# Kernel tuning notes

Measured on AMD Instinct MI355X. Metric: run time of the kernel, lower is better.

## Reference

```python
import jax, jax.numpy as jnp
import numpy as np

B, S, D = 1, 4096, 1024
H, Dh = 16, 64
F = 4096  # mlp_factor * D
EPS = 1e-6


def _ln(x, scale, bias=None):
    m = jnp.mean(x, axis=-1, keepdims=True)
    v = jnp.var(x, axis=-1, keepdims=True)
    y = (x - m) * jax.lax.rsqrt(v + EPS) * scale
    return y + bias if bias is not None else y


def setup_inputs() -> dict:
    key = jax.random.key(0)
    ks = jax.random.split(key, 10)
    lecun = lambda k, shape, fan_in: (jax.random.normal(k, shape, jnp.float32) * (fan_in ** -0.5))
    inp = {
        "x": jax.random.normal(ks[0], (B, S, D), jnp.float32),
        # causal mask, broadcastable to [B, H, S, S]
        "mask": jnp.tril(jnp.ones((S, S), bool))[None, None],
        # PreNorm (TPNorm -> LayerNorm)
        "ln_scale": jnp.ones((D,), jnp.float32),
        "ln_bias": jnp.zeros((D,), jnp.float32),
        # MLP input projection
        "w_in": lecun(ks[1], (D, F), D),
        "b_in": jnp.zeros((F,), jnp.float32),
        # QKV projection
        "wq": lecun(ks[2], (D, H, Dh), D),
        "bq": jnp.zeros((H, Dh), jnp.float32),
        "wk": lecun(ks[3], (D, H, Dh), D),
        "bk": jnp.zeros((H, Dh), jnp.float32),
        "wv": lecun(ks[4], (D, H, Dh), D),
        "bv": jnp.zeros((H, Dh), jnp.float32),
        # qk-norm scales (normalize_qk=True)
        "qn_scale": jnp.ones((Dh,), jnp.float32),
        "kn_scale": jnp.ones((Dh,), jnp.float32),
        # MLP output projection
        "w_mo": lecun(ks[5], (F, D), F),
        "b_mo": jnp.zeros((D,), jnp.float32),
        # Attention output projection
        "w_ao": lecun(ks[6], (H * Dh, D), H * Dh),
        "b_ao": jnp.zeros((D,), jnp.float32),
    }
    return inp


def reference(x, mask, ln_scale, ln_bias, w_in, b_in, wq, bq, wk, bk, wv, bv,
              qn_scale, kn_scale, w_mo, b_mo, w_ao, b_ao):
    residual = x
    xn = _ln(x, ln_scale, ln_bias)

    # fused QKV + MLP-input projections (QKVMLPDenseParallel)
    h = jax.nn.gelu(jnp.einsum("bsd,df->bsf", xn, w_in) + b_in)  # [B,S,F]
    q = jnp.einsum("bsd,dhk->bshk", xn, wq) + bq  # [B,S,H,Dh]
    k = jnp.einsum("bsd,dhk->bshk", xn, wk) + bk
    v = jnp.einsum("bsd,dhk->bshk", xn, wv) + bv
    # normalize_qk: per-head LayerNorm (no bias) on q, k
    q = _ln(q, qn_scale)
    k = _ln(k, kn_scale)

    # dot-product attention
    scores = jnp.einsum("bqhd,bkhd->bhqk", q, k) / np.sqrt(Dh).astype(np.float32)
    scores = jnp.where(mask, scores, jnp.finfo(scores.dtype).min)
    attn = jax.nn.softmax(scores, axis=-1)
    o = jnp.einsum("bhqk,bkhd->bqhd", attn, v)  # [B,S,H,Dh]

    # fused attention-out + MLP-out projections (AttnMLPOutParallel)
    mlp_out = jnp.einsum("bsf,fd->bsd", h, w_mo) + b_mo
    attn_out = jnp.einsum("bse,ed->bsd", o.reshape(B, S, H * Dh), w_ao) + b_ao

    # dropout deterministic (train=False); residual add
    return residual + mlp_out + attn_out
```

## Files before the change

kernel.cpp:

```cpp
#include <hip/hip_runtime.h>
#include <hip/hip_fp16.h>

typedef _Float16 half8 __attribute__((ext_vector_type(8)));
typedef float floatx4 __attribute__((ext_vector_type(4)));

constexpr int kS = 4096;
constexpr int kD = 1024;
constexpr int kH = 16;
constexpr int kDh = 64;
constexpr int kF = 4096;
constexpr int kNQKV = kF + 3 * kD;
constexpr int kKOut = kF + kD;

__device__ __forceinline__ void async_ld16(const void* g, void* l) {
  __builtin_amdgcn_global_load_lds(
      (const __attribute__((address_space(1))) void*)g,
      (__attribute__((address_space(3))) void*)l, 16, 0, 0);
}

#define CFENCE() asm volatile("" ::: "memory")

__global__ __launch_bounds__(256) void prep0_kernel(
    const float* __restrict__ w_in, const float* __restrict__ wq,
    const float* __restrict__ wk, const float* __restrict__ wv,
    const float* __restrict__ w_mo, const float* __restrict__ w_ao,
    _Float16* __restrict__ Wqkv, _Float16* __restrict__ Wout,
    const float* __restrict__ x, const float* __restrict__ ln_scale,
    const float* __restrict__ ln_bias, _Float16* __restrict__ xn) {
  __shared__ float t[32][33];
  __shared__ float red[8];
  int id = blockIdx.x;
  const int tid = threadIdx.x;

  if (id >= 12288) {
    const int row = id - 12288;
    const float* xr = x + (size_t)row * kD;
    float v[4];
    float s = 0.f, sq = 0.f;
#pragma unroll
    for (int i = 0; i < 4; ++i) {
      v[i] = xr[tid + 256 * i];
      s += v[i];
      sq += v[i] * v[i];
    }
    for (int off = 32; off; off >>= 1) {
      s += __shfl_xor(s, off);
      sq += __shfl_xor(sq, off);
    }
    const int wv2 = tid >> 6;
    if ((tid & 63) == 0) { red[wv2] = s; red[wv2 + 4] = sq; }
    __syncthreads();
    s = red[0] + red[1] + red[2] + red[3];
    sq = red[4] + red[5] + red[6] + red[7];
    const float mean = s * (1.0f / kD);
    const float var = sq * (1.0f / kD) - mean * mean;
    const float rstd = rsqrtf(var + 1e-6f);
#pragma unroll
    for (int i = 0; i < 4; ++i) {
      int d = tid + 256 * i;
      xn[(size_t)row * kD + d] = (_Float16)((v[i] - mean) * rstd * ln_scale[d] + ln_bias[d]);
    }
    return;
  }

  const float* src; _Float16* dst; int N, ldk, noff, koff, nt, kt;
  if (id < 4096)       { src = w_in; dst = Wqkv; N = kF; ldk = kD; noff = 0;        koff = 0;  nt = id & 127; kt = id >> 7; }
  else if (id < 5120)  { id -= 4096; src = wq;  dst = Wqkv; N = kD; ldk = kD; noff = kF;       koff = 0;  nt = id & 31; kt = id >> 5; }
  else if (id < 6144)  { id -= 5120; src = wk;  dst = Wqkv; N = kD; ldk = kD; noff = kF + kD;  koff = 0;  nt = id & 31; kt = id >> 5; }
  else if (id < 7168)  { id -= 6144; src = wv;  dst = Wqkv; N = kD; ldk = kD; noff = kF + 2*kD; koff = 0; nt = id & 31; kt = id >> 5; }
  else if (id < 11264) { id -= 7168; src = w_mo; dst = Wout; N = kD; ldk = kKOut; noff = 0;    koff = 0;  nt = id & 31; kt = id >> 5; }
  else                 { id -= 11264; src = w_ao; dst = Wout; N = kD; ldk = kKOut; noff = 0;   koff = kF; nt = id & 31; kt = id >> 5; }
  const int n0 = nt * 32, k0 = kt * 32;
#pragma unroll
  for (int i = 0; i < 4; ++i) {
    const int kl = (tid >> 5) + i * 8, nl = tid & 31;
    t[kl][nl] = src[(size_t)(k0 + kl) * N + n0 + nl];
  }
  __syncthreads();
#pragma unroll
  for (int i = 0; i < 4; ++i) {
    const int nl = (tid >> 5) + i * 8, kl = tid & 31;
    dst[(size_t)(noff + n0 + nl) * ldk + koff + k0 + kl] = (_Float16)t[kl][nl];
  }
}

__global__ __launch_bounds__(256) void htrans_kernel(
    const _Float16* __restrict__ src, _Float16* __restrict__ dst, int R, int C) {
  __shared__ _Float16 t[32][34];
  const int tid = threadIdx.x;
  const int c0 = blockIdx.x * 32, r0 = blockIdx.y * 32;
#pragma unroll
  for (int i = 0; i < 4; ++i) {
    const int rl = (tid >> 5) + i * 8, cl = tid & 31;
    t[rl][cl] = src[(size_t)(r0 + rl) * C + c0 + cl];
  }
  __syncthreads();
#pragma unroll
  for (int i = 0; i < 4; ++i) {
    const int cl = (tid >> 5) + i * 8, rl = tid & 31;
    dst[(size_t)(c0 + cl) * R + r0 + rl] = t[rl][cl];
  }
}

__device__ __forceinline__ float fast_gelu(float xv) {
  const float z = 0.7978845608028654f * (xv + 0.044715f * xv * xv * xv);
  const float u = exp2f(fminf(2.885390081777927f * z, 80.0f));
  return xv * u / (1.0f + u);
}

__global__ __launch_bounds__(512, 2) void gemm_qkvin(
    const _Float16* __restrict__ A, const _Float16* __restrict__ Bp,
    const float* __restrict__ b_in, const float* __restrict__ bq,
    const float* __restrict__ bk, const float* __restrict__ bv,
    const float* __restrict__ qn_scale, const float* __restrict__ kn_scale,
    _Float16* __restrict__ ho, _Float16* __restrict__ q,
    _Float16* __restrict__ k, _Float16* __restrict__ v) {
  __shared__ alignas(16) _Float16 Ts[65536];

  const int tid = threadIdx.x;
  const int lane = tid & 63;
  const int wave = tid >> 6;
  const int wr = wave >> 2;
  const int wc = wave & 3;
  const int lrow = lane & 15;
  const int quad = lane >> 4;

  int bid = blockIdx.y * 16 + blockIdx.x;
  bid = (bid & 7) * 56 + (bid >> 3);
  const int m0 = (bid & 15) * 256;
  const int n0 = (bid >> 4) * 256;

  const int swz = ((quad ^ (lrow & 3)) << 3);
  const int aoff = (wr * 128 + lrow) * 32 + swz;
  const int boff = 16384 + (wc * 64 + lrow) * 32 + swz;

  const int srow = wave * 32 + (lane >> 2);
  const int scol = (((lane & 3) ^ ((lane >> 2) & 3)) << 3);
  const int sldsl = wave * 1024;

  floatx4 acc[8][4] = {};

  auto stage = [&](int nb, int p, int kb) {
    const int mat = p & 1;
    const int lds0 = nb * 32768 + mat * 16384 + (p >> 1) * 8192 + sldsl;
    const _Float16* g0 = (mat == 0)
        ? A + (size_t)(m0 + srow) * kD + kb + scol
        : Bp + (size_t)(n0 + srow) * kD + kb + scol;
    async_ld16(g0, Ts + lds0);
    async_ld16(g0 + (size_t)16 * kD, Ts + lds0 + 512);
  };

  stage(0, 0, 0);
  stage(0, 1, 0);
  stage(0, 2, 32);
  stage(0, 3, 32);
  asm volatile("s_waitcnt vmcnt(4)" ::: "memory");
  CFENCE(); __builtin_amdgcn_s_barrier(); CFENCE();

  half8 af[8];
  constexpr int NT = kD / 64;
  for (int t = 0; t < NT; ++t) {
    const int cur = t & 1, nb = cur ^ 1;
    const int co = cur * 32768;
    const bool pf = (t + 1 < NT);
    const int kb1 = (t + 1) * 64;

    auto rdA = [&](int ks) {
#pragma unroll
      for (int mi = 0; mi < 8; ++mi)
        af[mi] = *reinterpret_cast<const half8*>(Ts + co + ks * 8192 + aoff + mi * 512);
    };
    auto rdB = [&](int ks, int nf) -> half8 {
      return *reinterpret_cast<const half8*>(Ts + co + ks * 8192 + boff + nf * 512);
    };
    half8 bf0, bf1;

    auto mm2 = [&](int nf0, half8 b0, half8 b1) {
      __builtin_amdgcn_s_setprio(1);
#pragma unroll
      for (int mi = 0; mi < 8; ++mi)
        acc[mi][nf0] = __builtin_amdgcn_mfma_f32_16x16x32_f16(af[mi], b0, acc[mi][nf0], 0, 0, 0);
#pragma unroll
      for (int mi = 0; mi < 8; ++mi)
        acc[mi][nf0 + 1] = __builtin_amdgcn_mfma_f32_16x16x32_f16(af[mi], b1, acc[mi][nf0 + 1], 0, 0, 0);
      __builtin_amdgcn_s_setprio(0);
    };

    rdA(0); bf0 = rdB(0, 0); bf1 = rdB(0, 1);
    if (pf) stage(nb, 0, kb1);
    CFENCE(); __builtin_amdgcn_s_barrier(); CFENCE();
    mm2(0, bf0, bf1);
    CFENCE(); __builtin_amdgcn_s_barrier(); CFENCE();

    bf0 = rdB(0, 2); bf1 = rdB(0, 3);
    if (pf) {
      stage(nb, 1, kb1);
      asm volatile("s_waitcnt vmcnt(4)" ::: "memory");
    } else {
      asm volatile("s_waitcnt vmcnt(0)" ::: "memory");
    }
    CFENCE(); __builtin_amdgcn_s_barrier(); CFENCE();
    mm2(2, bf0, bf1);
    CFENCE(); __builtin_amdgcn_s_barrier(); CFENCE();

    rdA(1); bf0 = rdB(1, 0); bf1 = rdB(1, 1);
    if (pf) stage(nb, 2, kb1 + 32);
    CFENCE(); __builtin_amdgcn_s_barrier(); CFENCE();
    mm2(0, bf0, bf1);
    CFENCE(); __builtin_amdgcn_s_barrier(); CFENCE();

    bf0 = rdB(1, 2); bf1 = rdB(1, 3);
    if (pf) {
      stage(nb, 3, kb1 + 32);
      asm volatile("s_waitcnt vmcnt(4)" ::: "memory");
    }
    CFENCE(); __builtin_amdgcn_s_barrier(); CFENCE();
    mm2(2, bf0, bf1);
    CFENCE(); __builtin_amdgcn_s_barrier(); CFENCE();
  }

  const int nblk0 = n0 + wc * 64;
  const int rbase = m0 + wr * 128 + quad * 4;

  if (nblk0 < kF) {
#pragma unroll
    for (int mi = 0; mi < 8; ++mi) {
      const int gm = rbase + mi * 16;
#pragma unroll
      for (int nf = 0; nf < 4; ++nf) {
        const int gn = nblk0 + nf * 16 + lrow;
        const float bn = b_in[gn];
#pragma unroll
        for (int r = 0; r < 4; ++r)
          ho[(size_t)(gm + r) * kKOut + gn] = (_Float16)fast_gelu(acc[mi][nf][r] + bn);
      }
    }
  } else if (nblk0 >= kF + 2 * kD) {
    const int cb = nblk0 - (kF + 2 * kD);
#pragma unroll
    for (int mi = 0; mi < 8; ++mi) {
      const int gm = rbase + mi * 16;
#pragma unroll
      for (int nf = 0; nf < 4; ++nf) {
        const int col = cb + nf * 16 + lrow;
        const float bn = bv[col];
#pragma unroll
        for (int r = 0; r < 4; ++r)
          v[(size_t)(gm + r) * kD + col] = (_Float16)(acc[mi][nf][r] + bn);
      }
    }
  } else {
    const bool isq = nblk0 < kF + kD;
    const float* nsc = isq ? qn_scale : kn_scale;
    const float* nb2 = isq ? bq : bk;
    const float sm = isq ? 0.18033688f : 1.0f;
    _Float16* dst = isq ? q : k;
    const int col0 = (nblk0 - kF) & (kD - 1);
    float bj[4];
#pragma unroll
    for (int nf = 0; nf < 4; ++nf) bj[nf] = nb2[col0 + nf * 16 + lrow];
#pragma unroll
    for (int mi = 0; mi < 8; ++mi) {
      const int gm = rbase + mi * 16;
#pragma unroll
      for (int r = 0; r < 4; ++r) {
        float vals[4], s1 = 0.f, s2 = 0.f;
#pragma unroll
        for (int nf = 0; nf < 4; ++nf) {
          const float vv = acc[mi][nf][r] + bj[nf];
          vals[nf] = vv; s1 += vv; s2 += vv * vv;
        }
#pragma unroll
        for (int off = 1; off <= 8; off <<= 1) {
          s1 += __shfl_xor(s1, off);
          s2 += __shfl_xor(s2, off);
        }
        const float mean = s1 * (1.0f / 64.0f);
        const float rstd = rsqrtf(s2 * (1.0f / 64.0f) - mean * mean + 1e-6f);
#pragma unroll
        for (int nf = 0; nf < 4; ++nf) {
          const int d = nf * 16 + lrow;
          dst[(size_t)(gm + r) * kD + col0 + d] =
              (_Float16)((vals[nf] - mean) * rstd * nsc[d] * sm);
        }
      }
    }
  }
}

__global__ __launch_bounds__(256) void prep_kernel(
    const float* __restrict__ x, const float* __restrict__ b_mo,
    const float* __restrict__ b_ao, float* __restrict__ out) {
  const int i = blockIdx.x * 256 + threadIdx.x;
  const int d = i & (kD - 1);
  out[i] = x[i] + b_mo[d] + b_ao[d];
}

__global__ __launch_bounds__(256) void gemm_out(
    const _Float16* __restrict__ A, const _Float16* __restrict__ Bp,
    float* __restrict__ out) {
  __shared__ alignas(16) _Float16 Ts[2][16 * 512];

  const int tid = threadIdx.x;
  const int lane = tid & 63;
  const int wave = tid >> 6;
  const int wm = (wave >> 1) * 64;
  const int wn = (wave & 1) * 64;
  const int m0 = blockIdx.x * 128;
  const int n0 = blockIdx.y * 128;
  const int kbeg = blockIdx.z * (kKOut / 2);
  const int kend = kbeg + kKOut / 2;
  const int lrow = lane & 15;
  const int quad = lane >> 4;

  floatx4 acc[4][4] = {};

  auto stage = [&](int buf, int k0) {
#pragma unroll
    for (int i = 0; i < 4; ++i) {
      const int chunk = wave * 4 + i;
      const int r = ((chunk & 7) << 4) + (lane >> 2);
      const int csrc = ((lane & 3) ^ ((r >> 1) & 3)) << 3;
      const _Float16* src = (chunk < 8)
          ? A + (size_t)(m0 + r) * kKOut + k0 + csrc
          : Bp + (size_t)(n0 + r) * kKOut + k0 + csrc;
      async_ld16(src, &Ts[buf][chunk * 512]);
    }
  };

  stage(0, kbeg);
  asm volatile("s_waitcnt vmcnt(0)" ::: "memory");
  __builtin_amdgcn_s_barrier();

  int cur = 0;
  for (int k0 = kbeg; k0 < kend; k0 += 32) {
    if (k0 + 32 < kend) stage(cur ^ 1, k0 + 32);

    const _Float16* As = Ts[cur];
    const _Float16* Bs = Ts[cur] + 8 * 512;
    half8 af[4], bf[4];
#pragma unroll
    for (int i = 0; i < 4; ++i) {
      const int ra = wm + i * 16 + lrow;
      const int rb = wn + i * 16 + lrow;
      af[i] = *reinterpret_cast<const half8*>(&As[ra * 32 + ((quad ^ ((ra >> 1) & 3)) << 3)]);
      bf[i] = *reinterpret_cast<const half8*>(&Bs[rb * 32 + ((quad ^ ((rb >> 1) & 3)) << 3)]);
    }
#pragma unroll
    for (int i = 0; i < 4; ++i)
#pragma unroll
      for (int j = 0; j < 4; ++j)
        acc[i][j] = __builtin_amdgcn_mfma_f32_16x16x32_f16(af[i], bf[j], acc[i][j], 0, 0, 0);

    asm volatile("s_waitcnt vmcnt(0)" ::: "memory");
    __builtin_amdgcn_s_barrier();
    cur ^= 1;
  }

#pragma unroll
  for (int i = 0; i < 4; ++i) {
    const int gm = m0 + wm + i * 16 + quad * 4;
#pragma unroll
    for (int j = 0; j < 4; ++j) {
      const int gn = n0 + wn + j * 16 + lrow;
#pragma unroll
      for (int r = 0; r < 4; ++r)
        atomicAdd(out + (size_t)(gm + r) * kD + gn, acc[i][j][r]);
    }
  }
}

__global__ __launch_bounds__(256) void fattn_kernel(
    const _Float16* __restrict__ Q, const _Float16* __restrict__ K,
    const _Float16* __restrict__ Vt, _Float16* __restrict__ ho) {
  __shared__ alignas(16) _Float16 Qs[64 * 64];
  __shared__ alignas(16) _Float16 Ks[64 * 64];
  __shared__ alignas(16) _Float16 Vs[64 * 64];
  __shared__ alignas(16) _Float16 Ps[64 * 72];

  const int tid = threadIdx.x;
  const int lane = tid & 63;
  const int wave = tid >> 6;
  const int lrow = lane & 15;
  const int quad = lane >> 4;
  const int qtile = 63 - blockIdx.x;
  const int h = blockIdx.y;
  const int qbase = qtile * 64;

  const int rs = lane >> 3;
  const int cs = lane & 7;

#pragma unroll
  for (int i = 0; i < 2; ++i) {
    const int chunk = wave * 2 + i;
    const int r = chunk * 8 + rs;
    async_ld16(Q + (size_t)(qbase + r) * kD + h * kDh + ((cs ^ (r & 7)) << 3),
               Qs + chunk * 512);
  }
  __syncthreads();

  half8 qf[2];
#pragma unroll
  for (int kt = 0; kt < 2; ++kt) {
    const int row = wave * 16 + lrow;
    qf[kt] = *reinterpret_cast<const half8*>(
        &Qs[row * 64 + (((kt * 4 + quad) ^ (row & 7)) << 3)]);
  }

  float lst[4] = {0.f, 0.f, 0.f, 0.f};
  floatx4 oacc[4] = {};
  const int qw = qbase + wave * 16;

  for (int t = 0; t <= qtile; ++t) {
    const int k0 = t * 64;
    __syncthreads();
#pragma unroll
    for (int i = 0; i < 4; ++i) {
      const int c2 = wave * 4 + i;
      if (c2 < 8) {
        const int r = c2 * 8 + rs;
        async_ld16(K + (size_t)(k0 + r) * kD + h * kDh + ((cs ^ (r & 7)) << 3),
                   Ks + c2 * 512);
      } else {
        const int c = c2 - 8;
        const int r = c * 8 + rs;
        async_ld16(Vt + (size_t)(h * kDh + r) * kS + k0 + ((cs ^ (r & 7)) << 3),
                   Vs + c * 512);
      }
    }
    __syncthreads();

    const bool diag = (t == qtile);

    floatx4 sacc[4] = {};
#pragma unroll
    for (int jt = 0; jt < 4; ++jt) {
      if (diag && jt > wave) continue;
#pragma unroll
      for (int kt = 0; kt < 2; ++kt) {
        const int rb = jt * 16 + lrow;
        half8 bfk = *reinterpret_cast<const half8*>(
            &Ks[rb * 64 + (((kt * 4 + quad) ^ (rb & 7)) << 3)]);
        sacc[jt] = __builtin_amdgcn_mfma_f32_16x16x32_f16(qf[kt], bfk, sacc[jt], 0, 0, 0);
      }
    }

    if (diag) {
#pragma unroll
      for (int jt = 0; jt < 4; ++jt) {
        const int kg = k0 + jt * 16 + lrow;
#pragma unroll
        for (int r = 0; r < 4; ++r)
          if (kg > qw + quad * 4 + r) sacc[jt][r] = -1e30f;
      }
    }

#pragma unroll
    for (int jt = 0; jt < 4; ++jt)
#pragma unroll
      for (int r = 0; r < 4; ++r) {
        const float p = exp2f(sacc[jt][r]);
        sacc[jt][r] = p;
        lst[r] += p;
      }

#pragma unroll
    for (int jt = 0; jt < 4; ++jt)
#pragma unroll
      for (int r = 0; r < 4; ++r)
        Ps[(wave * 16 + quad * 4 + r) * 72 + jt * 16 + lrow] = (_Float16)sacc[jt][r];

    const int ktmax = (diag && wave < 2) ? 1 : 2;
    for (int kt = 0; kt < ktmax; ++kt) {
      half8 pf = *reinterpret_cast<const half8*>(
          &Ps[(wave * 16 + lrow) * 72 + (kt * 4 + quad) * 8]);
#pragma unroll
      for (int jt = 0; jt < 4; ++jt) {
        const int rb = jt * 16 + lrow;
        half8 vf = *reinterpret_cast<const half8*>(
            &Vs[rb * 64 + (((kt * 4 + quad) ^ (rb & 7)) << 3)]);
        oacc[jt] = __builtin_amdgcn_mfma_f32_16x16x32_f16(pf, vf, oacc[jt], 0, 0, 0);
      }
    }
  }

#pragma unroll
  for (int r = 0; r < 4; ++r)
#pragma unroll
    for (int off = 8; off; off >>= 1) lst[r] += __shfl_xor(lst[r], off);
#pragma unroll
  for (int r = 0; r < 4; ++r) {
    const int qg = qw + quad * 4 + r;
    const float rcp = 1.0f / lst[r];
#pragma unroll
    for (int jt = 0; jt < 4; ++jt)
      ho[(size_t)qg * kKOut + kF + h * kDh + jt * 16 + lrow] =
          (_Float16)(oacc[jt][r] * rcp);
  }
}

extern "C" void kernel_launch(void* const* d_in, const int* in_sizes, int n_in,
                              void* d_out, int out_size, void* d_ws, size_t ws_size,
                              hipStream_t stream) {
  const float* x        = (const float*)d_in[0];
  const float* ln_scale = (const float*)d_in[2];
  const float* ln_bias  = (const float*)d_in[3];
  const float* w_in     = (const float*)d_in[4];
  const float* b_in     = (const float*)d_in[5];
  const float* wq       = (const float*)d_in[6];
  const float* bq       = (const float*)d_in[7];
  const float* wk       = (const float*)d_in[8];
  const float* bk       = (const float*)d_in[9];
  const float* wv       = (const float*)d_in[10];
  const float* bv       = (const float*)d_in[11];
  const float* qn_scale = (const float*)d_in[12];
  const float* kn_scale = (const float*)d_in[13];
  const float* w_mo     = (const float*)d_in[14];
  const float* b_mo     = (const float*)d_in[15];
  const float* w_ao     = (const float*)d_in[16];
  const float* b_ao     = (const float*)d_in[17];
  float* out = (float*)d_out;

  char* ws = (char*)d_ws;
  size_t off = 0;
  auto alloc = [&](size_t bytes) { char* p = ws + off; off += bytes; return p; };
  char* zone = (char*)alloc((size_t)kS * kD * 2 + (size_t)kNQKV * kD * 2);
  _Float16* xn   = (_Float16*)zone;
  _Float16* Wqkv = (_Float16*)(zone + (size_t)kS * kD * 2);
  _Float16* Wout = (_Float16*)alloc((size_t)kD * kKOut * 2);
  _Float16* ho   = (_Float16*)alloc((size_t)kS * kKOut * 2);
  _Float16* q_h  = (_Float16*)alloc((size_t)kS * kD * 2);
  _Float16* k_h  = (_Float16*)alloc((size_t)kS * kD * 2);
  _Float16* v_h  = (_Float16*)alloc((size_t)kS * kD * 2);
  _Float16* v_t  = (_Float16*)alloc((size_t)kS * kD * 2);

  prep0_kernel<<<12288 + 4096, 256, 0, stream>>>(
      w_in, wq, wk, wv, w_mo, w_ao, Wqkv, Wout, x, ln_scale, ln_bias, xn);

  gemm_qkvin<<<dim3(kS / 256, kNQKV / 256), 512, 0, stream>>>(
      xn, Wqkv, b_in, bq, bk, bv, qn_scale, kn_scale, ho, q_h, k_h, v_h);

  htrans_kernel<<<dim3(kD / 32, kS / 32), 256, 0, stream>>>(v_h, v_t, kS, kD);

  prep_kernel<<<kS * kD / 256, 256, 0, stream>>>(x, b_mo, b_ao, out);

  fattn_kernel<<<dim3(64, kH), 256, 0, stream>>>(q_h, k_h, v_t, ho);

  gemm_out<<<dim3(kS / 128, kD / 128, 2), 256, 0, stream>>>(ho, Wout, out);
}
```

Measured before the change: 491.0 us.

## Split attention KV loop across two blocks with paired query tiles and merge kernel

The attention kernel now pairs a short and a long causal query tile in each block so every block does a balanced amount of work. It also splits the key/value tiles by parity into two blocks along a new grid dimension, each writing unnormalized fp32 partial outputs and row sums. A new norm kernel adds the two partials, divides by the summed denominators and writes fp16 into the output projection input. A constant offset is subtracted before exp2 so the unnormalized sums stay in range. The aim is better load balance and more blocks to fill the GPU, at the cost of extra fp32 traffic, one more launch, and a dead workspace zone being reused.

```diff
diff --git a/kernel.cpp b/kernel.cpp
--- a/kernel.cpp
+++ b/kernel.cpp
@@ -372,7 +372,9 @@
 
 __global__ __launch_bounds__(256) void fattn_kernel(
     const _Float16* __restrict__ Q, const _Float16* __restrict__ K,
-    const _Float16* __restrict__ Vt, _Float16* __restrict__ ho) {
+    const _Float16* __restrict__ Vt, float* __restrict__ Oacc0,
+    float* __restrict__ Oacc1, float* __restrict__ Lacc0,
+    float* __restrict__ Lacc1) {
   __shared__ alignas(16) _Float16 Qs[64 * 64];
   __shared__ alignas(16) _Float16 Ks[64 * 64];
   __shared__ alignas(16) _Float16 Vs[64 * 64];
@@ -383,120 +385,139 @@
   const int wave = tid >> 6;
   const int lrow = lane & 15;
   const int quad = lane >> 4;
-  const int qtile = 63 - blockIdx.x;
   const int h = blockIdx.y;
-  const int qbase = qtile * 64;
+  const int pair = blockIdx.x;
+  const int split = blockIdx.z;
+  float* __restrict__ Oacc = split ? Oacc1 : Oacc0;
+  float* __restrict__ Lacc = split ? Lacc1 : Lacc0;
 
   const int rs = lane >> 3;
   const int cs = lane & 7;
-
-#pragma unroll
-  for (int i = 0; i < 2; ++i) {
-    const int chunk = wave * 2 + i;
-    const int r = chunk * 8 + rs;
-    async_ld16(Q + (size_t)(qbase + r) * kD + h * kDh + ((cs ^ (r & 7)) << 3),
-               Qs + chunk * 512);
-  }
-  __syncthreads();
-
-  half8 qf[2];
-#pragma unroll
-  for (int kt = 0; kt < 2; ++kt) {
-    const int row = wave * 16 + lrow;
-    qf[kt] = *reinterpret_cast<const half8*>(
-        &Qs[row * 64 + (((kt * 4 + quad) ^ (row & 7)) << 3)]);
-  }
-
-  float lst[4] = {0.f, 0.f, 0.f, 0.f};
-  floatx4 oacc[4] = {};
-  const int qw = qbase + wave * 16;
-
-  for (int t = 0; t <= qtile; ++t) {
-    const int k0 = t * 64;
+  constexpr float kOff = 11.5415603f;
+
+  for (int pass = 0; pass < 2; ++pass) {
+    const int qtile = pass ? (63 - pair) : pair;
+    const int qbase = qtile * 64;
+
     __syncthreads();
 #pragma unroll
-    for (int i = 0; i < 4; ++i) {
-      const int c2 = wave * 4 + i;
-      if (c2 < 8) {
-        const int r = c2 * 8 + rs;
-        async_ld16(K + (size_t)(k0 + r) * kD + h * kDh + ((cs ^ (r & 7)) << 3),
-                   Ks + c2 * 512);
-      } else {
-        const int c = c2 - 8;
-        const int r = c * 8 + rs;
-        async_ld16(Vt + (size_t)(h * kDh + r) * kS + k0 + ((cs ^ (r & 7)) << 3),
-                   Vs + c * 512);
-      }
+    for (int i = 0; i < 2; ++i) {
+      const int chunk = wave * 2 + i;
+      const int r = chunk * 8 + rs;
+      async_ld16(Q + (size_t)(qbase + r) * kD + h * kDh + ((cs ^ (r & 7)) << 3),
+                 Qs + chunk * 512);
     }
     __syncthreads();
 
-    const bool diag = (t == qtile);
-
-    floatx4 sacc[4] = {};
-#pragma unroll
-    for (int jt = 0; jt < 4; ++jt) {
-      if (diag && jt > wave) continue;
-#pragma unroll
-      for (int kt = 0; kt < 2; ++kt) {
-        const int rb = jt * 16 + lrow;
-        half8 bfk = *reinterpret_cast<const half8*>(
-            &Ks[rb * 64 + (((kt * 4 + quad) ^ (rb & 7)) << 3)]);
-        sacc[jt] = __builtin_amdgcn_mfma_f32_16x16x32_f16(qf[kt], bfk, sacc[jt], 0, 0, 0);
-      }
-    }
-
-    if (diag) {
+    half8 qf[2];
+#pragma unroll
+    for (int kt = 0; kt < 2; ++kt) {
+      const int row = wave * 16 + lrow;
+      qf[kt] = *reinterpret_cast<const half8*>(
+          &Qs[row * 64 + (((kt * 4 + quad) ^ (row & 7)) << 3)]);
+    }
+
+    float lst[4] = {0.f, 0.f, 0.f, 0.f};
+    floatx4 oacc[4] = {};
+    const int qw = qbase + wave * 16;
+
+    for (int t = split; t <= qtile; t += 2) {
+      const int k0 = t * 64;
+      __syncthreads();
+#pragma unroll
+      for (int i = 0; i < 4; ++i) {
+        const int c2 = wave * 4 + i;
+        if (c2 < 8) {
+          const int r = c2 * 8 + rs;
+          async_ld16(K + (size_t)(k0 + r) * kD + h * kDh + ((cs ^ (r & 7)) << 3),
+                     Ks + c2 * 512);
+        } else {
+          const int c = c2 - 8;
+          const int r = c * 8 + rs;
+          async_ld16(Vt + (size_t)(h * kDh + r) * kS + k0 + ((cs ^ (r & 7)) << 3),
+                     Vs + c * 512);
+        }
+      }
+      __syncthreads();
+
+      const bool diag = (t == qtile);
+
+      floatx4 sacc[4] = {};
 #pragma unroll
       for (int jt = 0; jt < 4; ++jt) {
-        const int kg = k0 + jt * 16 + lrow;
+        if (diag && jt > wave) continue;
+#pragma unroll
+        for (int kt = 0; kt < 2; ++kt) {
+          const int rb = jt * 16 + lrow;
+          half8 bfk = *reinterpret_cast<const half8*>(
+              &Ks[rb * 64 + (((kt * 4 + quad) ^ (rb & 7)) << 3)]);
+          sacc[jt] = __builtin_amdgcn_mfma_f32_16x16x32_f16(qf[kt], bfk, sacc[jt], 0, 0, 0);
+        }
+      }
+
+      if (diag) {
+#pragma unroll
+        for (int jt = 0; jt < 4; ++jt) {
+          const int kg = k0 + jt * 16 + lrow;
+#pragma unroll
+          for (int r = 0; r < 4; ++r)
+            if (kg > qw + quad * 4 + r) sacc[jt][r] = -1e30f;
+        }
+      }
+
+#pragma unroll
+      for (int jt = 0; jt < 4; ++jt)
+#pragma unroll
+        for (int r = 0; r < 4; ++r) {
+          const float p = exp2f(sacc[jt][r] - kOff);
+          sacc[jt][r] = p;
+          lst[r] += p;
+        }
+
+#pragma unroll
+      for (int jt = 0; jt < 4; ++jt)
 #pragma unroll
         for (int r = 0; r < 4; ++r)
-          if (kg > qw + quad * 4 + r) sacc[jt][r] = -1e30f;
-      }
-    }
-
-#pragma unroll
-    for (int jt = 0; jt < 4; ++jt)
-#pragma unroll
-      for (int r = 0; r < 4; ++r) {
-        const float p = exp2f(sacc[jt][r]);
-        sacc[jt][r] = p;
-        lst[r] += p;
-      }
-
-#pragma unroll
-    for (int jt = 0; jt < 4; ++jt)
-#pragma unroll
-      for (int r = 0; r < 4; ++r)
-        Ps[(wave * 16 + quad * 4 + r) * 72 + jt * 16 + lrow] = (_Float16)sacc[jt][r];
-
-    const int ktmax = (diag && wave < 2) ? 1 : 2;
-    for (int kt = 0; kt < ktmax; ++kt) {
-      half8 pf = *reinterpret_cast<const half8*>(
-          &Ps[(wave * 16 + lrow) * 72 + (kt * 4 + quad) * 8]);
-#pragma unroll
-      for (int jt = 0; jt < 4; ++jt) {
-        const int rb = jt * 16 + lrow;
-        half8 vf = *reinterpret_cast<const half8*>(
-            &Vs[rb * 64 + (((kt * 4 + quad) ^ (rb & 7)) << 3)]);
-        oacc[jt] = __builtin_amdgcn_mfma_f32_16x16x32_f16(pf, vf, oacc[jt], 0, 0, 0);
-      }
-    }
-  }
-
-#pragma unroll
-  for (int r = 0; r < 4; ++r)
-#pragma unroll
-    for (int off = 8; off; off >>= 1) lst[r] += __shfl_xor(lst[r], off);
-#pragma unroll
-  for (int r = 0; r < 4; ++r) {
-    const int qg = qw + quad * 4 + r;
-    const float rcp = 1.0f / lst[r];
-#pragma unroll
-    for (int jt = 0; jt < 4; ++jt)
-      ho[(size_t)qg * kKOut + kF + h * kDh + jt * 16 + lrow] =
-          (_Float16)(oacc[jt][r] * rcp);
-  }
+          Ps[(wave * 16 + quad * 4 + r) * 72 + jt * 16 + lrow] = (_Float16)sacc[jt][r];
+
+      const int ktmax = (diag && wave < 2) ? 1 : 2;
+      for (int kt = 0; kt < ktmax; ++kt) {
+        half8 pf = *reinterpret_cast<const half8*>(
+            &Ps[(wave * 16 + lrow) * 72 + (kt * 4 + quad) * 8]);
+#pragma unroll
+        for (int jt = 0; jt < 4; ++jt) {
+          const int rb = jt * 16 + lrow;
+          half8 vf = *reinterpret_cast<const half8*>(
+              &Vs[rb * 64 + (((kt * 4 + quad) ^ (rb & 7)) << 3)]);
+          oacc[jt] = __builtin_amdgcn_mfma_f32_16x16x32_f16(pf, vf, oacc[jt], 0, 0, 0);
+        }
+      }
+    }
+
+#pragma unroll
+    for (int r = 0; r < 4; ++r)
+#pragma unroll
+      for (int off = 8; off; off >>= 1) lst[r] += __shfl_xor(lst[r], off);
+#pragma unroll
+    for (int r = 0; r < 4; ++r) {
+      const int qg = qw + quad * 4 + r;
+      if (lrow == 0) Lacc[qg * kH + h] = lst[r];
+#pragma unroll
+      for (int jt = 0; jt < 4; ++jt)
+        Oacc[((size_t)qg * kH + h) * kDh + jt * 16 + lrow] = oacc[jt][r];
+    }
+  }
+}
+
+__global__ __launch_bounds__(256) void norm_kernel(
+    const float* __restrict__ Oacc0, const float* __restrict__ Oacc1,
+    const float* __restrict__ Lacc0, const float* __restrict__ Lacc1,
+    _Float16* __restrict__ ho) {
+  const int idx = blockIdx.x * 256 + threadIdx.x;
+  const int q = idx >> 10, rem = idx & 1023;
+  const int lidx = (q << 4) + (rem >> 6);
+  const float l = Lacc0[lidx] + Lacc1[lidx];
+  ho[(size_t)q * kKOut + kF + rem] = (_Float16)((Oacc0[idx] + Oacc1[idx]) / l);
 }
 
 extern "C" void kernel_launch(void* const* d_in, const int* in_sizes, int n_in,
@@ -527,12 +548,16 @@
   char* zone = (char*)alloc((size_t)kS * kD * 2 + (size_t)kNQKV * kD * 2);
   _Float16* xn   = (_Float16*)zone;
   _Float16* Wqkv = (_Float16*)(zone + (size_t)kS * kD * 2);
+  float* Oacc0 = (float*)zone;
+  float* Lacc0 = (float*)(zone + (size_t)kS * kD * 4);
+  float* Lacc1 = (float*)(zone + (size_t)kS * kD * 4 + (size_t)kS * kH * 4);
   _Float16* Wout = (_Float16*)alloc((size_t)kD * kKOut * 2);
   _Float16* ho   = (_Float16*)alloc((size_t)kS * kKOut * 2);
   _Float16* q_h  = (_Float16*)alloc((size_t)kS * kD * 2);
   _Float16* k_h  = (_Float16*)alloc((size_t)kS * kD * 2);
   _Float16* v_h  = (_Float16*)alloc((size_t)kS * kD * 2);
   _Float16* v_t  = (_Float16*)alloc((size_t)kS * kD * 2);
+  float* Oacc1   = (float*)alloc((size_t)kS * kD * 4);
 
   prep0_kernel<<<12288 + 4096, 256, 0, stream>>>(
       w_in, wq, wk, wv, w_mo, w_ao, Wqkv, Wout, x, ln_scale, ln_bias, xn);
@@ -544,7 +569,9 @@
 
   prep_kernel<<<kS * kD / 256, 256, 0, stream>>>(x, b_mo, b_ao, out);
 
-  fattn_kernel<<<dim3(64, kH), 256, 0, stream>>>(q_h, k_h, v_t, ho);
+  fattn_kernel<<<dim3(32, kH, 2), 256, 0, stream>>>(q_h, k_h, v_t, Oacc0, Oacc1, Lacc0, Lacc1);
+
+  norm_kernel<<<kS * kD / 256, 256, 0, stream>>>(Oacc0, Oacc1, Lacc0, Lacc1, ho);
 
   gemm_out<<<dim3(kS / 128, kD / 128, 2), 256, 0, stream>>>(ho, Wout, out);
 }
```

Result: faster. 443.5 us (-9.7%).
